# Optimization experiments

Hardware: AMD Instinct MI355X
Metric: run time of the kernel (lower is better)

## Reference

```python
import jax, jax.numpy as jnp
import numpy as np

B, R, S, C, H, MLP = 4, 32, 4, 128, 4, 512  # batch, resolution, box_size, dim, heads, mlp_dim
N = S ** 3            # tokens per window = 64
NW = (R // S) ** 3    # windows per batch element = 512
SHIFT = S // 2


def _layernorm(x, g, b):
    m = jnp.mean(x, axis=-1, keepdims=True)
    v = jnp.var(x, axis=-1, keepdims=True)
    return (x - m) * jax.lax.rsqrt(v + 1e-5) * g + b


def _box_partition(x):
    # x: (b, R, R, R, C) -> (b*NW, N, C)
    b = x.shape[0]
    x = x.reshape(b, R // S, S, R // S, S, R // S, S, C)
    x = x.transpose(0, 1, 3, 5, 2, 4, 6, 7)
    return x.reshape(-1, N, C)


def _box_reverse(w, b):
    # w: (b*NW, N, C) -> (b, R, R, R, C)
    x = w.reshape(b, R // S, R // S, R // S, S, S, S, C)
    x = x.transpose(0, 1, 4, 2, 5, 3, 6, 7)
    return x.reshape(b, R, R, R, C)


def setup_inputs():
    key = jax.random.key(0)
    ks = jax.random.split(key, 8)
    f = lambda k, sh: jax.random.normal(k, sh, dtype=jnp.float32) * 0.02
    x = jax.random.normal(ks[0], (B, R ** 3, C), dtype=jnp.float32)
    qkv_w = f(ks[1], (3 * C, C))
    rpb_table = f(ks[2], ((3 * S - 1) ** 3, H))
    proj_w = f(ks[3], (C, C))
    proj_b = jnp.zeros((C,), jnp.float32)
    norm1_g = jnp.ones((C,), jnp.float32)
    norm1_b = jnp.zeros((C,), jnp.float32)
    norm2_g = jnp.ones((C,), jnp.float32)
    norm2_b = jnp.zeros((C,), jnp.float32)
    mlp_w1 = f(ks[4], (MLP, C))
    mlp_b1 = jnp.zeros((MLP,), jnp.float32)
    mlp_w2 = f(ks[5], (C, MLP))
    mlp_b2 = jnp.zeros((C,), jnp.float32)
    # relative position index (N, N), int constant
    coords = np.stack(np.meshgrid(*([np.arange(S)] * 3), indexing='ij')).reshape(3, -1)
    rel = coords[:, :, None] - coords[:, None, :]
    rel = rel.transpose(1, 2, 0) + (S - 1)
    rel[..., 0] *= (2 * S - 1) ** 2
    rel[..., 1] *= (2 * S - 1)
    rel_index = jnp.asarray(rel.sum(-1), jnp.int32)
    # shifted-window additive attention mask (NW, N, N)
    img = np.zeros((1, R, R, R, 1), np.float32)
    sl = (slice(0, -S), slice(-S, -SHIFT), slice(-SHIFT, None))
    cnt = 0
    for a in sl:
        for b2 in sl:
            for c in sl:
                img[:, a, b2, c, :] = cnt
                cnt += 1
    m = img.reshape(1, R // S, S, R // S, S, R // S, S, 1)
    m = m.transpose(0, 1, 3, 5, 2, 4, 6, 7).reshape(-1, N)
    am = m[:, None, :] - m[:, :, None]
    attn_mask = jnp.asarray(np.where(am != 0, -100.0, 0.0).astype(np.float32))
    return dict(x=x, qkv_w=qkv_w, rpb_table=rpb_table, proj_w=proj_w, proj_b=proj_b,
                norm1_g=norm1_g, norm1_b=norm1_b, norm2_g=norm2_g, norm2_b=norm2_b,
                mlp_w1=mlp_w1, mlp_b1=mlp_b1, mlp_w2=mlp_w2, mlp_b2=mlp_b2,
                attn_mask=attn_mask, rel_index=rel_index)


def reference(x, qkv_w, rpb_table, proj_w, proj_b, norm1_g, norm1_b,
              norm2_g, norm2_b, mlp_w1, mlp_b1, mlp_w2, mlp_b2,
              attn_mask, rel_index):
    scale = (C // H) ** -0.5
    shortcut = x
    xn = _layernorm(x, norm1_g, norm1_b).reshape(B, R, R, R, C)
    xs = jnp.roll(xn, (-SHIFT,) * 3, axis=(1, 2, 3))
    w = _box_partition(xs)  # (B*NW, N, C)
    qkv = (w @ qkv_w.T).reshape(-1, N, 3, H, C // H).transpose(2, 0, 3, 1, 4)
    q, k, v = qkv[0] * scale, qkv[1], qkv[2]  # (B*NW, H, N, hd)
    attn = jnp.einsum('whnd,whmd->whnm', q, k)
    bias = rpb_table[rel_index].transpose(2, 0, 1)  # (H, N, N)
    attn = attn + bias[None]
    attn = attn.reshape(B, NW, H, N, N) + attn_mask[None, :, None]
    attn = jax.nn.softmax(attn.reshape(-1, H, N, N), axis=-1)
    out = jnp.einsum('whnm,whmd->whnd', attn, v).transpose(0, 2, 1, 3).reshape(-1, N, C)
    out = out @ proj_w.T + proj_b
    xm = _box_reverse(out, B)
    xm = jnp.roll(xm, (SHIFT,) * 3, axis=(1, 2, 3)).reshape(B, -1, C)
    x1 = shortcut + 0.5 * xm
    h = _layernorm(x1, norm2_g, norm2_b)
    h = jax.nn.gelu(h @ mlp_w1.T + mlp_b1, approximate=False) @ mlp_w2.T + mlp_b2
    return x1 + 0.5 * h
```

## Files before the change

### kernel.cpp

```cpp
#include <hip/hip_runtime.h>
#include <hip/hip_bf16.h>

typedef unsigned short u16;
typedef unsigned int u32;
typedef short bf16x8 __attribute__((ext_vector_type(8)));
typedef float f32x4 __attribute__((ext_vector_type(4)));

__device__ __forceinline__ u16 f2bf(float f) {
  union { float f; u32 i; } v; v.f = f;
  u32 x = v.i;
  x += 0x7fff + ((x >> 16) & 1);
  return (u16)(x >> 16);
}
__device__ __forceinline__ u32 pack2(float a, float b) {
  return (u32)f2bf(a) | ((u32)f2bf(b) << 16);
}
__device__ __forceinline__ u32 cvtpk2(float a, float b) {
  __hip_bfloat162 t = __float22bfloat162_rn(float2{a, b});
  union { __hip_bfloat162 h; u32 u; } v; v.h = t; return v.u;
}


__global__ void prep_kernel(const float* __restrict__ rpb, const int* __restrict__ rel,
                            const float* __restrict__ qkv_w, const float* __restrict__ proj_w,
                            const float* __restrict__ w1, const float* __restrict__ w2,
                            float* __restrict__ bias, u16* __restrict__ qkv_f,
                            u16* __restrict__ proj_f, u16* __restrict__ w1f,
                            u16* __restrict__ w2f) {
  const int bid = blockIdx.x;
  if (bid < 64) {
    const int idx = bid * 256 + threadIdx.x;
    const int h = idx >> 12, rm = idx & 4095;
    bias[idx] = rpb[rel[rm] * 4 + h];
    return;
  }
  const int i4 = (bid - 64) * 256 + threadIdx.x;
  const int e = i4 * 4;
  const float scale = 0.17677669529663687f;
  float4 v; u16* dst;
  if (e < 49152) {
    v = *(const float4*)(qkv_w + e);
    if (e < 16384) { v.x *= scale; v.y *= scale; v.z *= scale; v.w *= scale; }
    const int row = e >> 7, col = e & 127;
    const int tile = (row >> 4) * 4 + (col >> 5);
    const int lane = ((col >> 3) & 3) * 16 + (row & 15);
    dst = qkv_f + tile * 512 + lane * 8 + (col & 7);
  } else if (e < 65536) {
    const int le = e - 49152;
    v = *(const float4*)(proj_w + le);
    const int row = le >> 7, col = le & 127;
    const int tile = (row >> 4) * 4 + (col >> 5);
    const int lane = ((col >> 3) & 3) * 16 + (row & 15);
    dst = proj_f + tile * 512 + lane * 8 + (col & 7);
  } else if (e < 131072) {
    const int le = e - 65536;
    v = *(const float4*)(w1 + le);
    const int row = le >> 7, col = le & 127;
    const int tile = (row >> 4) * 4 + (col >> 5);
    const int lane = ((col >> 3) & 3) * 16 + (row & 15);
    dst = w1f + tile * 512 + lane * 8 + (col & 7);
  } else {
    const int le = e - 131072;
    v = *(const float4*)(w2 + le);
    const int row = le >> 9, col = le & 511;
    const int tile = (row >> 4) * 16 + (col >> 5);
    const int lane = ((col >> 3) & 3) * 16 + (row & 15);
    dst = w2f + tile * 512 + lane * 8 + (col & 7);
  }
  *(uint2*)dst = make_uint2(pack2(v.x, v.y), pack2(v.z, v.w));
}

__global__ __launch_bounds__(512, 4) void fused_kernel(
    const float* __restrict__ x, const u16* __restrict__ qkv_f,
    const u16* __restrict__ proj_f, const float* __restrict__ proj_b,
    const float* __restrict__ n1g, const float* __restrict__ n1b,
    const float* __restrict__ amask, const float* __restrict__ bias,
    const u16* __restrict__ w1f, const float* __restrict__ b1,
    const u16* __restrict__ w2f, const float* __restrict__ b2,
    const float* __restrict__ n2g, const float* __restrict__ n2b,
    float* __restrict__ out)
{
  __shared__ __align__(16) unsigned char lds[70656];
  __shared__ int srcIdx[64];
  u16* xw = (u16*)(lds);
  u16* qb = (u16*)(lds + 17408);
  u16* kb = (u16*)(lds + 34816);
  u16* vt = (u16*)(lds + 52224);
  unsigned char* Pb = lds;
  u16* Ob = kb;
  float* x1f = (float*)(lds);
  u16* xn  = (u16*)(lds + 34816);
  u16* h1c0 = (u16*)(lds + 52224);
  u16* h1c1 = (u16*)(lds + 61440);

  const int tid = threadIdx.x;
  const int wv = tid >> 6, lane = tid & 63;
  const int l15 = lane & 15, lg = lane >> 4;
  const int hw = wv & 3;
  const int half = wv >> 2;

  const int wIdx = blockIdx.x;
  const int bb = wIdx >> 9, ww = wIdx & 511;
  const int w0 = ww >> 6, w1i = (ww >> 3) & 7, w2i = ww & 7;

  {
    const int tok = tid >> 3;
    const int qt = tid & 7;
    const int s0 = tok >> 4, s1 = (tok >> 2) & 3, s2 = tok & 3;
    const int p0 = (w0 * 4 + s0 + 2) & 31;
    const int p1 = (w1i * 4 + s1 + 2) & 31;
    const int p2 = (w2i * 4 + s2 + 2) & 31;
    const int src = (bb << 15) + (p0 << 10) + (p1 << 5) + p2;
    if (qt == 0) srcIdx[tok] = src;
    float v[16]; float s = 0.f, sq = 0.f;
    const float4* p4 = (const float4*)(x + src * 128 + qt * 16);
    #pragma unroll
    for (int i = 0; i < 4; ++i) {
      float4 u = p4[i];
      v[i * 4 + 0] = u.x; v[i * 4 + 1] = u.y; v[i * 4 + 2] = u.z; v[i * 4 + 3] = u.w;
      s += u.x + u.y + u.z + u.w;
      sq += u.x * u.x + u.y * u.y + u.z * u.z + u.w * u.w;
    }
    s  += __shfl_xor(s, 1);  s  += __shfl_xor(s, 2);  s  += __shfl_xor(s, 4);
    sq += __shfl_xor(sq, 1); sq += __shfl_xor(sq, 2); sq += __shfl_xor(sq, 4);
    const float mean = s * 0.0078125f;
    const float var  = sq * 0.0078125f - mean * mean;
    const float rstd = rsqrtf(var + 1e-5f);
    u16* dst = xw + tok * 136 + qt * 16;
    #pragma unroll
    for (int i = 0; i < 16; i += 2) {
      const int c = qt * 16 + i;
      float y0 = (v[i]     - mean) * rstd * n1g[c]     + n1b[c];
      float y1 = (v[i + 1] - mean) * rstd * n1g[c + 1] + n1b[c + 1];
      *(u32*)(dst + i) = cvtpk2(y0, y1);
    }
  }
  __syncthreads();

  const f32x4 zero4 = {0.f, 0.f, 0.f, 0.f};

  bf16x8 xa[2][4];
  #pragma unroll
  for (int ti = 0; ti < 2; ++ti)
    #pragma unroll
    for (int ks = 0; ks < 4; ++ks)
      xa[ti][ks] = *(const bf16x8*)(xw + ((half * 2 + ti) * 16 + l15) * 136 + ks * 32 + lg * 8);

  #pragma unroll
  for (int cc = 0; cc < 4; ++cc) {
    const u16* wp = qkv_f + (cc * 4 + hw) * 4 * 512 + lane * 8;
    f32x4 acc[2] = {zero4, zero4};
    #pragma unroll
    for (int ks = 0; ks < 4; ++ks) {
      const bf16x8 bfr = *(const bf16x8*)(wp + ks * 512);
      acc[0] = __builtin_amdgcn_mfma_f32_16x16x32_bf16(bfr, xa[0][ks], acc[0], 0, 0, 0);
      acc[1] = __builtin_amdgcn_mfma_f32_16x16x32_bf16(bfr, xa[1][ks], acc[1], 0, 0, 0);
    }
    u16* dstbuf = (cc < 2) ? qb : kb;
    const int ob = (cc & 1) * 64 + hw * 16 + lg * 4;
    #pragma unroll
    for (int ti = 0; ti < 2; ++ti) {
      const int token = (half * 2 + ti) * 16 + l15;
      uint2 pk = make_uint2(cvtpk2(acc[ti][0], acc[ti][1]), cvtpk2(acc[ti][2], acc[ti][3]));
      *(uint2*)(dstbuf + token * 136 + ob) = pk;
    }
  }
  #pragma unroll
  for (int cc = 4; cc < 6; ++cc) {
    const u16* wp = qkv_f + (cc * 4 + hw) * 4 * 512 + lane * 8;
    f32x4 acc[2] = {zero4, zero4};
    #pragma unroll
    for (int ks = 0; ks < 4; ++ks) {
      const bf16x8 bfr = *(const bf16x8*)(wp + ks * 512);
      acc[0] = __builtin_amdgcn_mfma_f32_16x16x32_bf16(xa[0][ks], bfr, acc[0], 0, 0, 0);
      acc[1] = __builtin_amdgcn_mfma_f32_16x16x32_bf16(xa[1][ks], bfr, acc[1], 0, 0, 0);
    }
    const int cvch = (cc - 4) * 64 + hw * 16 + l15;
    #pragma unroll
    for (int ti = 0; ti < 2; ++ti) {
      uint2 pk = make_uint2(cvtpk2(acc[ti][0], acc[ti][1]), cvtpk2(acc[ti][2], acc[ti][3]));
      *(uint2*)(vt + cvch * 72 + (half * 2 + ti) * 16 + lg * 4) = pk;
    }
  }
  __syncthreads();

  f32x4 s[2][4];
  {
    bf16x8 qa[2];
    #pragma unroll
    for (int ti = 0; ti < 2; ++ti)
      qa[ti] = *(const bf16x8*)(qb + ((half * 2 + ti) * 16 + l15) * 136 + hw * 32 + lg * 8);
    #pragma unroll
    for (int tj = 0; tj < 4; ++tj) {
      const bf16x8 kf = *(const bf16x8*)(kb + (tj * 16 + l15) * 136 + hw * 32 + lg * 8);
      s[0][tj] = __builtin_amdgcn_mfma_f32_16x16x32_bf16(qa[0], kf, zero4, 0, 0, 0);
      s[1][tj] = __builtin_amdgcn_mfma_f32_16x16x32_bf16(qa[1], kf, zero4, 0, 0, 0);
    }
  }
  #pragma unroll
  for (int ti = 0; ti < 2; ++ti) {
    #pragma unroll
    for (int r = 0; r < 4; ++r) {
      const int row = (half * 2 + ti) * 16 + lg * 4 + r;
      const float* bp = bias + hw * 4096 + row * 64;
      const float* mp = amask + ww * 4096 + row * 64;
      #pragma unroll
      for (int tj = 0; tj < 4; ++tj) {
        const int col = tj * 16 + l15;
        s[ti][tj][r] += bp[col] + mp[col];
      }
    }
  }
  __syncthreads();

  unsigned char* ps = Pb + wv * 4096;
  #pragma unroll
  for (int ti = 0; ti < 2; ++ti) {
    #pragma unroll
    for (int r = 0; r < 4; ++r) {
      float mx = fmaxf(fmaxf(s[ti][0][r], s[ti][1][r]), fmaxf(s[ti][2][r], s[ti][3][r]));
      mx = fmaxf(mx, __shfl_xor(mx, 1));
      mx = fmaxf(mx, __shfl_xor(mx, 2));
      mx = fmaxf(mx, __shfl_xor(mx, 4));
      mx = fmaxf(mx, __shfl_xor(mx, 8));
      float sum = 0.f;
      #pragma unroll
      for (int tj = 0; tj < 4; ++tj) {
        float e = __expf(s[ti][tj][r] - mx);
        s[ti][tj][r] = e; sum += e;
      }
      sum += __shfl_xor(sum, 1);
      sum += __shfl_xor(sum, 2);
      sum += __shfl_xor(sum, 4);
      sum += __shfl_xor(sum, 8);
      const float rcp = 1.0f / sum;
      const int row = ti * 16 + lg * 4 + r;
      const int swz = (row & 7) << 4;
      #pragma unroll
      for (int tj = 0; tj < 4; ++tj) {
        const int byteoff = (row * 128 + (tj * 16 + l15) * 2) ^ swz;
        *(u16*)(ps + byteoff) = f2bf(s[ti][tj][r] * rcp);
      }
    }
  }

  {
    f32x4 oacc[2][2] = {{zero4, zero4}, {zero4, zero4}};
    #pragma unroll
    for (int ks = 0; ks < 2; ++ks) {
      bf16x8 pa[2], vb[2];
      #pragma unroll
      for (int ti = 0; ti < 2; ++ti) {
        const int row = ti * 16 + l15;
        const int slot = ((ks * 4 + lg) ^ (row & 7)) << 4;
        pa[ti] = *(const bf16x8*)(ps + row * 128 + slot);
      }
      #pragma unroll
      for (int tj = 0; tj < 2; ++tj)
        vb[tj] = *(const bf16x8*)(vt + (hw * 32 + tj * 16 + l15) * 72 + ks * 32 + lg * 8);
      #pragma unroll
      for (int ti = 0; ti < 2; ++ti)
        #pragma unroll
        for (int tj = 0; tj < 2; ++tj)
          oacc[ti][tj] = __builtin_amdgcn_mfma_f32_16x16x32_bf16(vb[tj], pa[ti], oacc[ti][tj], 0, 0, 0);
    }
    #pragma unroll
    for (int ti = 0; ti < 2; ++ti)
      #pragma unroll
      for (int tj = 0; tj < 2; ++tj) {
        const int token = (half * 2 + ti) * 16 + l15;
        uint2 pk = make_uint2(cvtpk2(oacc[ti][tj][0], oacc[ti][tj][1]),
                              cvtpk2(oacc[ti][tj][2], oacc[ti][tj][3]));
        *(uint2*)(Ob + token * 136 + hw * 32 + tj * 16 + lg * 4) = pk;
      }
  }
  __syncthreads();

  bf16x8 oafr[2][4];
  #pragma unroll
  for (int ti = 0; ti < 2; ++ti)
    #pragma unroll
    for (int ks = 0; ks < 4; ++ks)
      oafr[ti][ks] = *(const bf16x8*)(Ob + ((half * 2 + ti) * 16 + l15) * 136 + ks * 32 + lg * 8);
  #pragma unroll
  for (int cc = 0; cc < 2; ++cc) {
    const u16* wp = proj_f + (cc * 4 + hw) * 4 * 512 + lane * 8;
    f32x4 acc[2] = {zero4, zero4};
    #pragma unroll
    for (int ks = 0; ks < 4; ++ks) {
      const bf16x8 bfr = *(const bf16x8*)(wp + ks * 512);
      acc[0] = __builtin_amdgcn_mfma_f32_16x16x32_bf16(bfr, oafr[0][ks], acc[0], 0, 0, 0);
      acc[1] = __builtin_amdgcn_mfma_f32_16x16x32_bf16(bfr, oafr[1][ks], acc[1], 0, 0, 0);
    }
    const int cb = cc * 64 + hw * 16 + lg * 4;
    const float4 pb4 = *(const float4*)(proj_b + cb);
    #pragma unroll
    for (int ti = 0; ti < 2; ++ti) {
      const int token = (half * 2 + ti) * 16 + l15;
      const int src = srcIdx[token];
      float4 xr = *(const float4*)(x + src * 128 + cb);
      xr.x += 0.5f * (acc[ti][0] + pb4.x);
      xr.y += 0.5f * (acc[ti][1] + pb4.y);
      xr.z += 0.5f * (acc[ti][2] + pb4.z);
      xr.w += 0.5f * (acc[ti][3] + pb4.w);
      *(float4*)(x1f + token * 132 + cb) = xr;
    }
  }
  __syncthreads();

  {
    const int tok = tid >> 3;
    const int qt = tid & 7;
    float v[16]; float s2 = 0.f, sq = 0.f;
    const float4* p4 = (const float4*)(x1f + tok * 132 + qt * 16);
    #pragma unroll
    for (int i = 0; i < 4; ++i) {
      float4 u = p4[i];
      v[i * 4 + 0] = u.x; v[i * 4 + 1] = u.y; v[i * 4 + 2] = u.z; v[i * 4 + 3] = u.w;
      s2 += u.x + u.y + u.z + u.w;
      sq += u.x * u.x + u.y * u.y + u.z * u.z + u.w * u.w;
    }
    s2 += __shfl_xor(s2, 1); s2 += __shfl_xor(s2, 2); s2 += __shfl_xor(s2, 4);
    sq += __shfl_xor(sq, 1); sq += __shfl_xor(sq, 2); sq += __shfl_xor(sq, 4);
    const float mean = s2 * 0.0078125f;
    const float var  = sq * 0.0078125f - mean * mean;
    const float rstd = rsqrtf(var + 1e-5f);
    u16* dst = xn + tok * 136 + qt * 16;
    #pragma unroll
    for (int i = 0; i < 16; i += 2) {
      const int c = qt * 16 + i;
      float y0 = (v[i]     - mean) * rstd * n2g[c]     + n2b[c];
      float y1 = (v[i + 1] - mean) * rstd * n2g[c + 1] + n2b[c + 1];
      *(u32*)(dst + i) = cvtpk2(y0, y1);
    }
  }
  __syncthreads();

  f32x4 acc2[2][2] = {{zero4, zero4}, {zero4, zero4}};
  #pragma unroll 1
  for (int oc = 0; oc < 8; ++oc) {
    u16* h1c = (oc & 1) ? h1c1 : h1c0;
    f32x4 a1[2] = {zero4, zero4};
    const u16* wp1 = w1f + (oc * 4 + hw) * 4 * 512 + lane * 8;
    #pragma unroll
    for (int ks = 0; ks < 4; ++ks) {
      const bf16x8 bfr = *(const bf16x8*)(wp1 + ks * 512);
      #pragma unroll
      for (int ti = 0; ti < 2; ++ti) {
        const bf16x8 afr = *(const bf16x8*)(xn + ((half * 2 + ti) * 16 + l15) * 136 + ks * 32 + lg * 8);
        a1[ti] = __builtin_amdgcn_mfma_f32_16x16x32_bf16(bfr, afr, a1[ti], 0, 0, 0);
      }
    }
    bf16x8 w2r[2][2];
    #pragma unroll
    for (int tj = 0; tj < 2; ++tj)
      #pragma unroll
      for (int ks = 0; ks < 2; ++ks)
        w2r[tj][ks] = *(const bf16x8*)(w2f + (((hw * 2 + tj) * 16) + (oc * 2 + ks)) * 512 + lane * 8);

    const int olb = hw * 16 + lg * 4;
    const float4 b14 = *(const float4*)(b1 + oc * 64 + olb);
    const float b1v[4] = {b14.x, b14.y, b14.z, b14.w};
    #pragma unroll
    for (int ti = 0; ti < 2; ++ti) {
      float g[4];
      #pragma unroll
      for (int r = 0; r < 4; ++r) {
        const float u = a1[ti][r] + b1v[r];
        const float t = u + 0.044715f * u * u * u;
        g[r] = u / (1.0f + __expf(-1.5957691216057308f * t));
      }
      const int token = (half * 2 + ti) * 16 + l15;
      *(uint2*)(h1c + token * 72 + olb) = make_uint2(cvtpk2(g[0], g[1]), cvtpk2(g[2], g[3]));
    }
    __syncthreads();

    #pragma unroll
    for (int ks = 0; ks < 2; ++ks) {
      bf16x8 afr[2];
      #pragma unroll
      for (int ti = 0; ti < 2; ++ti)
        afr[ti] = *(const bf16x8*)(h1c + ((half * 2 + ti) * 16 + l15) * 72 + ks * 32 + lg * 8);
      #pragma unroll
      for (int ti = 0; ti < 2; ++ti)
        #pragma unroll
        for (int tj = 0; tj < 2; ++tj)
          acc2[ti][tj] = __builtin_amdgcn_mfma_f32_16x16x32_bf16(w2r[tj][ks], afr[ti], acc2[ti][tj], 0, 0, 0);
    }
  }

  #pragma unroll
  for (int tj = 0; tj < 2; ++tj) {
    const int cb = hw * 32 + tj * 16 + lg * 4;
    const float4 b24 = *(const float4*)(b2 + cb);
    #pragma unroll
    for (int ti = 0; ti < 2; ++ti) {
      const int token = (half * 2 + ti) * 16 + l15;
      const int src = srcIdx[token];
      float4 xr = *(const float4*)(x1f + token * 132 + cb);
      xr.x += 0.5f * (acc2[ti][tj][0] + b24.x);
      xr.y += 0.5f * (acc2[ti][tj][1] + b24.y);
      xr.z += 0.5f * (acc2[ti][tj][2] + b24.z);
      xr.w += 0.5f * (acc2[ti][tj][3] + b24.w);
      *(float4*)(out + src * 128 + cb) = xr;
    }
  }
}

extern "C" void kernel_launch(void* const* d_in, const int* in_sizes, int n_in,
                              void* d_out, int out_size, void* d_ws, size_t ws_size,
                              hipStream_t stream) {
  const float* x      = (const float*)d_in[0];
  const float* qkv_w  = (const float*)d_in[1];
  const float* rpb    = (const float*)d_in[2];
  const float* proj_w = (const float*)d_in[3];
  const float* proj_b = (const float*)d_in[4];
  const float* n1g    = (const float*)d_in[5];
  const float* n1b    = (const float*)d_in[6];
  const float* n2g    = (const float*)d_in[7];
  const float* n2b    = (const float*)d_in[8];
  const float* w1     = (const float*)d_in[9];
  const float* b1     = (const float*)d_in[10];
  const float* w2     = (const float*)d_in[11];
  const float* b2     = (const float*)d_in[12];
  const float* amask  = (const float*)d_in[13];
  const int*   rel    = (const int*)d_in[14];
  float* out  = (float*)d_out;

  unsigned char* ws = (unsigned char*)d_ws;
  float* bias = (float*)(ws);
  u16* qkv_f  = (u16*)(ws + 65536);
  u16* proj_f = (u16*)(ws + 163840);
  u16* w1f    = (u16*)(ws + 196608);
  u16* w2f    = (u16*)(ws + 327680);

  prep_kernel<<<256, 256, 0, stream>>>(rpb, rel, qkv_w, proj_w, w1, w2,
                                       bias, qkv_f, proj_f, w1f, w2f);
  fused_kernel<<<2048, 512, 0, stream>>>(x, qkv_f, proj_f, proj_b, n1g, n1b, amask, bias,
                                         w1f, b1, w2f, b2, n2g, n2b, out);
}
```

Baseline: 146.1 us.

## Fold log2e into scales, skip mask on interior windows, drop softmax max

```diff
diff --git a/kernel.cpp b/kernel.cpp
--- a/kernel.cpp
+++ b/kernel.cpp
@@ -19,24 +19,32 @@
   __hip_bfloat162 t = __float22bfloat162_rn(float2{a, b});
   union { __hip_bfloat162 h; u32 u; } v; v.h = t; return v.u;
 }
+__device__ __forceinline__ float fastrcp(float x) {
+  float r;
+  asm("v_rcp_f32 %0, %1" : "=v"(r) : "v"(x));
+  return r;
+}
+
+#define L2E 1.4426950408889634f
 
 
 __global__ void prep_kernel(const float* __restrict__ rpb, const int* __restrict__ rel,
                             const float* __restrict__ qkv_w, const float* __restrict__ proj_w,
                             const float* __restrict__ w1, const float* __restrict__ w2,
-                            float* __restrict__ bias, u16* __restrict__ qkv_f,
+                            float* __restrict__ bias_t, u16* __restrict__ qkv_f,
                             u16* __restrict__ proj_f, u16* __restrict__ w1f,
                             u16* __restrict__ w2f) {
   const int bid = blockIdx.x;
   if (bid < 64) {
     const int idx = bid * 256 + threadIdx.x;
     const int h = idx >> 12, rm = idx & 4095;
-    bias[idx] = rpb[rel[rm] * 4 + h];
+    const int r = rm >> 6, c = rm & 63;
+    bias_t[h * 4096 + c * 64 + r] = rpb[rel[rm] * 4 + h] * L2E;
     return;
   }
   const int i4 = (bid - 64) * 256 + threadIdx.x;
   const int e = i4 * 4;
-  const float scale = 0.17677669529663687f;
+  const float scale = 0.17677669529663687f * L2E;
   float4 v; u16* dst;
   if (e < 49152) {
     v = *(const float4*)(qkv_w + e);
@@ -74,7 +82,7 @@
     const float* __restrict__ x, const u16* __restrict__ qkv_f,
     const u16* __restrict__ proj_f, const float* __restrict__ proj_b,
     const float* __restrict__ n1g, const float* __restrict__ n1b,
-    const float* __restrict__ amask, const float* __restrict__ bias,
+    const float* __restrict__ amask, const float* __restrict__ bias_t,
     const u16* __restrict__ w1f, const float* __restrict__ b1,
     const u16* __restrict__ w2f, const float* __restrict__ b2,
     const float* __restrict__ n2g, const float* __restrict__ n2b,
@@ -102,6 +110,7 @@
   const int wIdx = blockIdx.x;
   const int bb = wIdx >> 9, ww = wIdx & 511;
   const int w0 = ww >> 6, w1i = (ww >> 3) & 7, w2i = ww & 7;
+  const bool hasMask = (w0 == 7) || (w1i == 7) || (w2i == 7);
 
   {
     const int tok = tid >> 3;
@@ -199,47 +208,52 @@
   }
   #pragma unroll
   for (int ti = 0; ti < 2; ++ti) {
+    const int rowb = (half * 2 + ti) * 16 + lg * 4;
+    #pragma unroll
+    for (int tj = 0; tj < 4; ++tj) {
+      const int col = tj * 16 + l15;
+      const float4 bt = *(const float4*)(bias_t + hw * 4096 + col * 64 + rowb);
+      s[ti][tj][0] += bt.x; s[ti][tj][1] += bt.y;
+      s[ti][tj][2] += bt.z; s[ti][tj][3] += bt.w;
+    }
+  }
+  if (hasMask) {
+    #pragma unroll
+    for (int ti = 0; ti < 2; ++ti) {
+      #pragma unroll
+      for (int r = 0; r < 4; ++r) {
+        const int row = (half * 2 + ti) * 16 + lg * 4 + r;
+        const float* mp = amask + ww * 4096 + row * 64;
+        #pragma unroll
+        for (int tj = 0; tj < 4; ++tj)
+          s[ti][tj][r] = fmaf(mp[tj * 16 + l15], L2E, s[ti][tj][r]);
+      }
+    }
+  }
+  __syncthreads();
+
+  unsigned char* ps = Pb + wv * 4096;
+  #pragma unroll
+  for (int ti = 0; ti < 2; ++ti) {
     #pragma unroll
     for (int r = 0; r < 4; ++r) {
-      const int row = (half * 2 + ti) * 16 + lg * 4 + r;
-      const float* bp = bias + hw * 4096 + row * 64;
-      const float* mp = amask + ww * 4096 + row * 64;
+      float e[4]; float sum = 0.f;
       #pragma unroll
       for (int tj = 0; tj < 4; ++tj) {
-        const int col = tj * 16 + l15;
-        s[ti][tj][r] += bp[col] + mp[col];
-      }
-    }
-  }
-  __syncthreads();
-
-  unsigned char* ps = Pb + wv * 4096;
-  #pragma unroll
-  for (int ti = 0; ti < 2; ++ti) {
-    #pragma unroll
-    for (int r = 0; r < 4; ++r) {
-      float mx = fmaxf(fmaxf(s[ti][0][r], s[ti][1][r]), fmaxf(s[ti][2][r], s[ti][3][r]));
-      mx = fmaxf(mx, __shfl_xor(mx, 1));
-      mx = fmaxf(mx, __shfl_xor(mx, 2));
-      mx = fmaxf(mx, __shfl_xor(mx, 4));
-      mx = fmaxf(mx, __shfl_xor(mx, 8));
-      float sum = 0.f;
-      #pragma unroll
-      for (int tj = 0; tj < 4; ++tj) {
-        float e = __expf(s[ti][tj][r] - mx);
-        s[ti][tj][r] = e; sum += e;
+        e[tj] = exp2f(s[ti][tj][r]);
+        sum += e[tj];
       }
       sum += __shfl_xor(sum, 1);
       sum += __shfl_xor(sum, 2);
       sum += __shfl_xor(sum, 4);
       sum += __shfl_xor(sum, 8);
-      const float rcp = 1.0f / sum;
+      const float rcp = fastrcp(sum);
       const int row = ti * 16 + lg * 4 + r;
       const int swz = (row & 7) << 4;
       #pragma unroll
       for (int tj = 0; tj < 4; ++tj) {
         const int byteoff = (row * 128 + (tj * 16 + l15) * 2) ^ swz;
-        *(u16*)(ps + byteoff) = f2bf(s[ti][tj][r] * rcp);
+        *(u16*)(ps + byteoff) = f2bf(e[tj] * rcp);
       }
     }
   }
@@ -368,7 +382,7 @@
       for (int r = 0; r < 4; ++r) {
         const float u = a1[ti][r] + b1v[r];
         const float t = u + 0.044715f * u * u * u;
-        g[r] = u / (1.0f + __expf(-1.5957691216057308f * t));
+        g[r] = u * fastrcp(1.0f + exp2f(-2.302207725f * t));
       }
       const int token = (half * 2 + ti) * 16 + l15;
       *(uint2*)(h1c + token * 72 + olb) = make_uint2(cvtpk2(g[0], g[1]), cvtpk2(g[2], g[3]));
@@ -428,14 +442,14 @@
   float* out  = (float*)d_out;
 
   unsigned char* ws = (unsigned char*)d_ws;
-  float* bias = (float*)(ws);
+  float* bias_t = (float*)(ws);
   u16* qkv_f  = (u16*)(ws + 65536);
   u16* proj_f = (u16*)(ws + 163840);
   u16* w1f    = (u16*)(ws + 196608);
   u16* w2f    = (u16*)(ws + 327680);
 
   prep_kernel<<<256, 256, 0, stream>>>(rpb, rel, qkv_w, proj_w, w1, w2,
-                                       bias, qkv_f, proj_f, w1f, w2f);
-  fused_kernel<<<2048, 512, 0, stream>>>(x, qkv_f, proj_f, proj_b, n1g, n1b, amask, bias,
+                                       bias_t, qkv_f, proj_f, w1f, w2f);
+  fused_kernel<<<2048, 512, 0, stream>>>(x, qkv_f, proj_f, proj_b, n1g, n1b, amask, bias_t,
                                          w1f, b1, w2f, b2, n2g, n2b, out);
 }
```

Result: no change. 144.1 us (-1.4%).
